# Performance work log

Hardware: AMD Instinct MI355X
Metric: run time of the kernel (lower is better)

The kernel has to match this reference:

```python
import jax, jax.numpy as jnp
import numpy as np

B, IN_DIM, T = 4, 512, 4096
EMBED, HEADS, NB_FEAT = 1024, 16, 256
D_HEAD = EMBED // HEADS
EPS = 1e-6


def _orthogonal_random_matrix(key, nb_rows, nb_cols):
    # scaling==1 branch: sqrt(nb_cols) * Q from reduced QR of a Gaussian block
    block = jax.random.normal(key, (nb_rows, nb_cols), dtype=jnp.float32)
    q, _ = jnp.linalg.qr(block)
    return jnp.sqrt(jnp.float32(nb_cols)) * q


def setup_inputs() -> dict:
    key = jax.random.key(0)
    kx, kq, kk, kv, ko, kp = jax.random.split(key, 6)
    s = 1.0 / np.sqrt(IN_DIM)
    return {
        "x": jax.random.normal(kx, (B, IN_DIM, T), dtype=jnp.float32),
        "Wq": jax.random.normal(kq, (IN_DIM, EMBED), dtype=jnp.float32) * s,
        "Wk": jax.random.normal(kk, (IN_DIM, EMBED), dtype=jnp.float32) * s,
        "Wv": jax.random.normal(kv, (IN_DIM, EMBED), dtype=jnp.float32) * s,
        "Wo": jax.random.normal(ko, (EMBED, EMBED), dtype=jnp.float32) * (1.0 / np.sqrt(EMBED)),
        "proj": _orthogonal_random_matrix(kp, NB_FEAT, D_HEAD),
    }


def reference(x, Wq, Wk, Wv, Wo, proj):
    b, c, t = x.shape
    x_bt = jnp.transpose(x, (0, 2, 1))  # (B, T, in_dim)
    Q = (x_bt @ Wq).reshape(b, t, HEADS, D_HEAD)
    K = (x_bt @ Wk).reshape(b, t, HEADS, D_HEAD)
    V = (x_bt @ Wv).reshape(b, t, HEADS, D_HEAD)
    # exponential random-feature map
    Qp = jnp.exp(jnp.einsum('bthd,fd->bthf', Q, proj)) + EPS
    Kp = jnp.exp(jnp.einsum('bthd,fd->bthf', K, proj)) + EPS
    K_sum = Kp.sum(axis=1)                              # (B, H, F)
    KV = jnp.einsum('bthf,bthd->bhfd', Kp, V)           # (B, H, F, D)
    denom = jnp.maximum(jnp.einsum('bthf,bhf->bth', Qp, K_sum), 1e-6)
    numer = jnp.einsum('bthf,bhfd->bthd', Qp, KV)
    attn = numer / denom[..., None]                     # (B, T, H, D)
    out2 = attn.reshape(b, t, HEADS * D_HEAD) @ Wo      # (B, T, embed)
    cat = jnp.concatenate([x_bt, out2], axis=-1)        # (B, T, in_dim+embed)
    return jnp.transpose(cat, (0, 2, 1))
```

## Files before the change

### kernel.cpp

```cpp
#include <hip/hip_runtime.h>


constexpr int kB  = 4;
constexpr int kIn = 512;
constexpr int kT  = 4096;
constexpr int kE  = 1024;
constexpr int kH  = 16;
constexpr int kD  = 64;
constexpr int kF  = 256;
constexpr int kQKVs = 3072;

typedef __attribute__((ext_vector_type(8))) short bf16x8;
typedef __attribute__((ext_vector_type(4))) float f32x4;

__device__ __forceinline__ unsigned short f2bf(float f) {
    unsigned u = __float_as_uint(f);
    u += 0x7fff + ((u >> 16) & 1);
    return (unsigned short)(u >> 16);
}
__device__ __forceinline__ float bf2f(unsigned short s) {
    return __uint_as_float(((unsigned)s) << 16);
}
__device__ __forceinline__ void gload_lds16(const void* g, void* l) {
    __builtin_amdgcn_global_load_lds((const __attribute__((address_space(1))) void*)g,
                                     (__attribute__((address_space(3))) void*)l, 16, 0, 0);
}

__global__ __launch_bounds__(256) void zero_kernel(float* __restrict__ p, int n) {
    int i = blockIdx.x * 256 + threadIdx.x;
    if (i < n) p[i] = 0.f;
}

__global__ __launch_bounds__(256) void copy_x_kernel(const float* __restrict__ x,
                                                     float* __restrict__ out) {
    const int perB4 = kIn * kT / 4;
    int idx = blockIdx.x * 256 + threadIdx.x;
    if (idx < kB * perB4) {
        int b = idx / perB4, e = idx % perB4;
        ((float4*)out)[(size_t)b * ((kIn + kE) * kT / 4) + e] = ((const float4*)x)[idx];
    }
}

__global__ __launch_bounds__(256) void f2b_flat_kernel(const float* __restrict__ s,
                                                       unsigned short* __restrict__ d, int n4) {
    int i = blockIdx.x * 256 + threadIdx.x;
    if (i < n4) {
        float4 v = ((const float4*)s)[i];
        ushort4 o;
        o.x = f2bf(v.x); o.y = f2bf(v.y); o.z = f2bf(v.z); o.w = f2bf(v.w);
        ((ushort4*)d)[i] = o;
    }
}

__global__ __launch_bounds__(256) void trans_f2b_kernel(const float* __restrict__ src,
                                                        unsigned short* __restrict__ dst,
                                                        int R, int C,
                                                        long sstride, long dstride) {
    __shared__ float L[64][68];
    src += (size_t)blockIdx.z * sstride;
    dst += (size_t)blockIdx.z * dstride;
    const int c0 = blockIdx.x * 64, r0 = blockIdx.y * 64;
    const int tid = threadIdx.x;
#pragma unroll
    for (int it = 0; it < 4; ++it) {
        int lin = it * 256 + tid;
        int i = lin >> 4;
        int j4 = (lin & 15) * 4;
        float4 v = *(const float4*)(src + (size_t)(r0 + i) * C + c0 + j4);
        L[j4 + 0][i] = v.x; L[j4 + 1][i] = v.y; L[j4 + 2][i] = v.z; L[j4 + 3][i] = v.w;
    }
    __syncthreads();
#pragma unroll
    for (int it = 0; it < 4; ++it) {
        int lin = it * 256 + tid;
        int cc = lin >> 4;
        int r4 = (lin & 15) * 4;
        ushort4 o;
        o.x = f2bf(L[cc][r4 + 0]); o.y = f2bf(L[cc][r4 + 1]);
        o.z = f2bf(L[cc][r4 + 2]); o.w = f2bf(L[cc][r4 + 3]);
        *(ushort4*)(dst + (size_t)(c0 + cc) * R + r0 + r4) = o;
    }
}

__global__ __launch_bounds__(256) void trans_qkv_kernel(const float* __restrict__ Wq,
                                                        const float* __restrict__ Wk,
                                                        const float* __restrict__ Wv,
                                                        unsigned short* __restrict__ dst) {
    __shared__ float L[64][68];
    const int z = blockIdx.z;
    const float* src = (z == 0) ? Wq : (z == 1) ? Wk : Wv;
    dst += (size_t)z * kE * kIn;
    const int c0 = blockIdx.x * 64, r0 = blockIdx.y * 64;
    const int tid = threadIdx.x;
#pragma unroll
    for (int it = 0; it < 4; ++it) {
        int lin = it * 256 + tid;
        int i = lin >> 4;
        int j4 = (lin & 15) * 4;
        float4 v = *(const float4*)(src + (size_t)(r0 + i) * kE + c0 + j4);
        L[j4 + 0][i] = v.x; L[j4 + 1][i] = v.y; L[j4 + 2][i] = v.z; L[j4 + 3][i] = v.w;
    }
    __syncthreads();
#pragma unroll
    for (int it = 0; it < 4; ++it) {
        int lin = it * 256 + tid;
        int cc = lin >> 4;
        int r4 = (lin & 15) * 4;
        ushort4 o;
        o.x = f2bf(L[cc][r4 + 0]); o.y = f2bf(L[cc][r4 + 1]);
        o.z = f2bf(L[cc][r4 + 2]); o.w = f2bf(L[cc][r4 + 3]);
        *(ushort4*)(dst + (size_t)(c0 + cc) * kIn + r0 + r4) = o;
    }
}

__device__ __forceinline__ void stage256(const unsigned short* __restrict__ A,
                                         const unsigned short* __restrict__ Bt,
                                         int K, int m0, int n0, int kt,
                                         unsigned short* AsB, unsigned short* BsB,
                                         int tid) {
    const int w = tid >> 6;
    const size_t k0 = (size_t)kt * 64;
#pragma unroll
    for (int r = 0; r < 4; ++r) {
        int idx = r * 512 + tid;
        int row = idx >> 3;
        int cg = (idx & 7) ^ (row & 7);
        gload_lds16(A + (size_t)(m0 + row) * K + k0 + cg * 8, AsB + r * 4096 + w * 512);
    }
#pragma unroll
    for (int r = 0; r < 4; ++r) {
        int idx = r * 512 + tid;
        int row = idx >> 3;
        int cg = (idx & 7) ^ (row & 7);
        gload_lds16(Bt + (size_t)(n0 + row) * K + k0 + cg * 8, BsB + r * 4096 + w * 512);
    }
}

__device__ __forceinline__ void gemm256_mainloop(const unsigned short* __restrict__ A,
                                                 const unsigned short* __restrict__ Bt,
                                                 int K, int m0, int n0,
                                                 unsigned short* smem,
                                                 f32x4 (&acc)[8][4]) {
    const int tid = threadIdx.x, lane = tid & 63, w = tid >> 6;
    const int col = lane & 15, quad = lane >> 4;
    const int wm = (w >> 2) * 128, wn = (w & 3) * 64;
    const int swz = col & 7;
    const int nt = K >> 6;
    unsigned short* As0 = smem;
    unsigned short* As1 = smem + 16384;
    unsigned short* Bs0 = smem + 32768;
    unsigned short* Bs1 = smem + 49152;

    stage256(A, Bt, K, m0, n0, 0, As0, Bs0, tid);
    stage256(A, Bt, K, m0, n0, 1, As1, Bs1, tid);
#pragma unroll
    for (int i = 0; i < 8; ++i)
#pragma unroll
        for (int j = 0; j < 4; ++j) acc[i][j] = (f32x4){0.f, 0.f, 0.f, 0.f};
    asm volatile("s_waitcnt vmcnt(8)" ::: "memory");
    __builtin_amdgcn_s_barrier();
    __builtin_amdgcn_sched_barrier(0);

    for (int t = 0; ; ++t) {
        const unsigned short* As_ = (t & 1) ? As1 : As0;
        const unsigned short* Bs_ = (t & 1) ? Bs1 : Bs0;
#pragma unroll
        for (int q = 0; q < 4; ++q) {
            const int ar0 = wm + (q >> 1) * 64;
            const int bc0 = wn + (q & 1) * 32;
            bf16x8 av[2][4], bv[2][2];
#pragma unroll
            for (int s = 0; s < 2; ++s) {
                const int kc = ((s * 4 + quad) ^ swz) * 8;
#pragma unroll
                for (int i = 0; i < 4; ++i)
                    av[s][i] = *(const bf16x8*)&As_[(ar0 + i * 16 + col) * 64 + kc];
#pragma unroll
                for (int j = 0; j < 2; ++j)
                    bv[s][j] = *(const bf16x8*)&Bs_[(bc0 + j * 16 + col) * 64 + kc];
            }
            __builtin_amdgcn_s_setprio(1);
#pragma unroll
            for (int s = 0; s < 2; ++s)
#pragma unroll
                for (int i = 0; i < 4; ++i)
#pragma unroll
                    for (int j = 0; j < 2; ++j)
                        acc[(q >> 1) * 4 + i][(q & 1) * 2 + j] =
                            __builtin_amdgcn_mfma_f32_16x16x32_bf16(
                                av[s][i], bv[s][j],
                                acc[(q >> 1) * 4 + i][(q & 1) * 2 + j], 0, 0, 0);
            __builtin_amdgcn_s_setprio(0);
            __builtin_amdgcn_sched_barrier(0);
            __builtin_amdgcn_s_barrier();
            __builtin_amdgcn_sched_barrier(0);
        }
        if (t == nt - 1) break;
        if (t + 2 < nt) {
            stage256(A, Bt, K, m0, n0, t + 2, (t & 1) ? As1 : As0, (t & 1) ? Bs1 : Bs0, tid);
            asm volatile("s_waitcnt vmcnt(8)" ::: "memory");
        } else {
            asm volatile("s_waitcnt vmcnt(0)" ::: "memory");
        }
        __builtin_amdgcn_sched_barrier(0);
        __builtin_amdgcn_s_barrier();
        __builtin_amdgcn_sched_barrier(0);
    }
}

__global__ __launch_bounds__(512) void gemm256_b16(const unsigned short* __restrict__ A,
                                                   const unsigned short* __restrict__ Bt,
                                                   unsigned short* __restrict__ C,
                                                   int N, int K, int ntN) {
    extern __shared__ unsigned short smem_us[];
    const int tid = threadIdx.x, lane = tid & 63, w = tid >> 6;
    const int col = lane & 15, quad = lane >> 4;
    const int wm = (w >> 2) * 128, wn = (w & 3) * 64;
    const int bid = blockIdx.x;
    const int qch = gridDim.x >> 3;
    const int swb = (bid & 7) * qch + (bid >> 3);
    const int mt = swb / ntN, ntl = swb - mt * ntN;
    const int m0 = mt * 256, n0 = ntl * 256;

    f32x4 acc[8][4];
    gemm256_mainloop(A, Bt, K, m0, n0, smem_us, acc);

    float* Tw = (float*)smem_us + w * 336;
    const int t2 = lane >> 2, n4 = (lane & 3) * 4;
#pragma unroll
    for (int ri = 0; ri < 8; ++ri)
#pragma unroll
        for (int cj = 0; cj < 4; ++cj) {
#pragma unroll
            for (int r = 0; r < 4; ++r)
                Tw[(quad * 4 + r) * 20 + col] = acc[ri][cj][r];
            float4 v = *(const float4*)&Tw[t2 * 20 + n4];
            ushort4 o;
            o.x = f2bf(v.x); o.y = f2bf(v.y); o.z = f2bf(v.z); o.w = f2bf(v.w);
            *(ushort4*)(C + (size_t)(m0 + wm + ri * 16 + t2) * N + n0 + wn + cj * 16 + n4) = o;
        }
}

__global__ __launch_bounds__(512) void gemm256_out(const unsigned short* __restrict__ A,
                                                   const unsigned short* __restrict__ Bt,
                                                   float* __restrict__ out,
                                                   int N, int K, int ntN) {
    extern __shared__ unsigned short smem_us[];
    const int tid = threadIdx.x, lane = tid & 63, w = tid >> 6;
    const int col = lane & 15, quad = lane >> 4;
    const int wm = (w >> 2) * 128, wn = (w & 3) * 64;
    const int bid = blockIdx.x;
    const int qch = gridDim.x >> 3;
    const int swb = (bid & 7) * qch + (bid >> 3);
    const int mt = swb / ntN, ntl = swb - mt * ntN;
    const int m0 = mt * 256, n0 = ntl * 256;

    f32x4 acc[8][4];
    gemm256_mainloop(A, Bt, K, m0, n0, smem_us, acc);

    const int b = m0 >> 12, t0 = m0 & 4095;
    float* dst = out + (size_t)b * (kIn + kE) * kT + (size_t)kIn * kT;
    float* Tw = (float*)smem_us + w * 336;
    const int n2 = lane >> 2, t4 = (lane & 3) * 4;
#pragma unroll
    for (int ri = 0; ri < 8; ++ri)
#pragma unroll
        for (int cj = 0; cj < 4; ++cj) {
            *(float4*)&Tw[col * 20 + quad * 4] =
                (float4){acc[ri][cj][0], acc[ri][cj][1], acc[ri][cj][2], acc[ri][cj][3]};
            float4 v = *(const float4*)&Tw[n2 * 20 + t4];
            *(float4*)(dst + (size_t)(n0 + wn + cj * 16 + n2) * kT + t0 + wm + ri * 16 + t4) = v;
        }
}

__global__ __launch_bounds__(256) void phaseA_mfma(const unsigned short* __restrict__ QKVb,
                                                   const unsigned short* __restrict__ projb,
                                                   float* __restrict__ KVg,
                                                   float* __restrict__ Ksumg) {
    __shared__ unsigned short Ks[64 * 64];
    __shared__ unsigned short VT[64 * 72];
    __shared__ unsigned short KpT[256 * 72];
    const int tid = threadIdx.x, lane = tid & 63, w = tid >> 6;
    const int col = lane & 15, quad = lane >> 4;
    const int bh = blockIdx.x, b = bh >> 4, h = bh & 15;
    const int grp = blockIdx.y;
    const int f0 = w * 64;
    const int swz = col & 7;

    bf16x8 bB[2][4];
#pragma unroll
    for (int s = 0; s < 2; ++s)
#pragma unroll
        for (int j = 0; j < 4; ++j)
            bB[s][j] = *(const bf16x8*)(projb + (size_t)(f0 + j * 16 + col) * 64 + s * 32 + quad * 8);

    f32x4 kvacc[4][4];
#pragma unroll
    for (int i = 0; i < 4; ++i)
#pragma unroll
        for (int j = 0; j < 4; ++j) kvacc[i][j] = (f32x4){0.f, 0.f, 0.f, 0.f};
    float ksum_acc[4] = {0.f, 0.f, 0.f, 0.f};

    for (int it = 0; it < 8; ++it) {
        const size_t rowbase = (size_t)(b * kT + grp * 512 + it * 64) * kQKVs + h * kD;
        __syncthreads();
#pragma unroll
        for (int i2 = 0; i2 < 2; ++i2) {
            int p = (i2 * 4 + w) * 64 + lane;
            int row = p >> 3;
            int cg = ((p & 7) ^ (row & 7)) * 8;
            gload_lds16(QKVb + rowbase + 1024 + (size_t)row * kQKVs + cg, &Ks[(i2 * 4 + w) * 512]);
        }
#pragma unroll
        for (int r = 0; r < 4; ++r) {
            int lin = r * 256 + tid;
            int t = lin >> 4, d4 = (lin & 15) * 4;
            ushort4 v = *(const ushort4*)(QKVb + rowbase + 2048 + (size_t)t * kQKVs + d4);
            VT[(d4 + 0) * 72 + t] = v.x; VT[(d4 + 1) * 72 + t] = v.y;
            VT[(d4 + 2) * 72 + t] = v.z; VT[(d4 + 3) * 72 + t] = v.w;
        }
        __syncthreads();
        bf16x8 av[2][4];
#pragma unroll
        for (int s = 0; s < 2; ++s)
#pragma unroll
            for (int i = 0; i < 4; ++i)
                av[s][i] = *(const bf16x8*)&Ks[(i * 16 + col) * 64 + ((s * 4 + quad) ^ swz) * 8];
#pragma unroll
        for (int j = 0; j < 4; ++j) {
            f32x4 sa[4];
#pragma unroll
            for (int i = 0; i < 4; ++i) sa[i] = (f32x4){0.f, 0.f, 0.f, 0.f};
#pragma unroll
            for (int s = 0; s < 2; ++s)
#pragma unroll
                for (int i = 0; i < 4; ++i)
                    sa[i] = __builtin_amdgcn_mfma_f32_16x16x32_bf16(av[s][i], bB[s][j], sa[i], 0, 0, 0);
            const int f = f0 + j * 16 + col;
#pragma unroll
            for (int i = 0; i < 4; ++i) {
                float e0 = __expf(sa[i][0]) + 1e-6f;
                float e1 = __expf(sa[i][1]) + 1e-6f;
                float e2 = __expf(sa[i][2]) + 1e-6f;
                float e3 = __expf(sa[i][3]) + 1e-6f;
                ksum_acc[j] += (e0 + e1) + (e2 + e3);
                ushort4 pk;
                pk.x = f2bf(e0); pk.y = f2bf(e1); pk.z = f2bf(e2); pk.w = f2bf(e3);
                *(ushort4*)&KpT[f * 72 + i * 16 + quad * 4] = pk;
            }
        }
#pragma unroll
        for (int s = 0; s < 2; ++s) {
            const int kc = s * 32 + quad * 8;
            bf16x8 a2[4], b2[4];
#pragma unroll
            for (int i = 0; i < 4; ++i)
                a2[i] = *(const bf16x8*)&KpT[(f0 + i * 16 + col) * 72 + kc];
#pragma unroll
            for (int jn = 0; jn < 4; ++jn)
                b2[jn] = *(const bf16x8*)&VT[(jn * 16 + col) * 72 + kc];
#pragma unroll
            for (int i = 0; i < 4; ++i)
#pragma unroll
                for (int jn = 0; jn < 4; ++jn)
                    kvacc[i][jn] = __builtin_amdgcn_mfma_f32_16x16x32_bf16(a2[i], b2[jn], kvacc[i][jn], 0, 0, 0);
        }
    }
    const size_t kvbase = (size_t)bh * (kF * kD);
#pragma unroll
    for (int i = 0; i < 4; ++i)
#pragma unroll
        for (int jn = 0; jn < 4; ++jn)
#pragma unroll
            for (int r = 0; r < 4; ++r)
                atomicAdd(&KVg[kvbase + (size_t)(f0 + i * 16 + quad * 4 + r) * kD + jn * 16 + col],
                          kvacc[i][jn][r]);
#pragma unroll
    for (int j = 0; j < 4; ++j) {
        float v = ksum_acc[j];
        v += __shfl_xor(v, 16);
        v += __shfl_xor(v, 32);
        if (quad == 0) atomicAdd(&Ksumg[(size_t)bh * kF + f0 + j * 16 + col], v);
    }
}

__global__ __launch_bounds__(256) void phaseB_mfma(const unsigned short* __restrict__ QKVb,
                                                   const unsigned short* __restrict__ projb,
                                                   const unsigned short* __restrict__ KVTb,
                                                   const float* __restrict__ Ksumg,
                                                   unsigned short* __restrict__ attnb) {
    __shared__ unsigned short Qs[64 * 64];
    __shared__ unsigned short Qp[64 * 264];
    __shared__ unsigned short KVTs[64 * 264];
    __shared__ float KsS[256];
    __shared__ float denp[4][64];
    const int tid = threadIdx.x, lane = tid & 63, w = tid >> 6;
    const int col = lane & 15, quad = lane >> 4;
    const int bh = blockIdx.x, b = bh >> 4, h = bh & 15;
    const int grp = blockIdx.y;
    const int f0 = w * 64;
    const int swz = col & 7;

    bf16x8 bB[2][4];
#pragma unroll
    for (int s = 0; s < 2; ++s)
#pragma unroll
        for (int j = 0; j < 4; ++j)
            bB[s][j] = *(const bf16x8*)(projb + (size_t)(f0 + j * 16 + col) * 64 + s * 32 + quad * 8);

#pragma unroll
    for (int r = 0; r < 8; ++r) {
        int lin = r * 256 + tid;
        int d = lin >> 5, fc8 = (lin & 31) * 8;
        *(bf16x8*)&KVTs[d * 264 + fc8] = *(const bf16x8*)(KVTb + (size_t)bh * 16384 + d * 256 + fc8);
    }
    KsS[tid] = Ksumg[(size_t)bh * kF + tid];

    for (int it = 0; it < 8; ++it) {
        const int tg0 = grp * 512 + it * 64;
        const size_t rowbase = (size_t)(b * kT + tg0) * kQKVs + h * kD;
        __syncthreads();
#pragma unroll
        for (int i2 = 0; i2 < 2; ++i2) {
            int p = (i2 * 4 + w) * 64 + lane;
            int row = p >> 3;
            int cg = ((p & 7) ^ (row & 7)) * 8;
            gload_lds16(QKVb + rowbase + (size_t)row * kQKVs + cg, &Qs[(i2 * 4 + w) * 512]);
        }
        __syncthreads();
        bf16x8 av[2][4];
#pragma unroll
        for (int s = 0; s < 2; ++s)
#pragma unroll
            for (int i = 0; i < 4; ++i)
                av[s][i] = *(const bf16x8*)&Qs[(i * 16 + col) * 64 + ((s * 4 + quad) ^ swz) * 8];
#pragma unroll
        for (int j = 0; j < 4; ++j) {
            f32x4 sa[4];
#pragma unroll
            for (int i = 0; i < 4; ++i) sa[i] = (f32x4){0.f, 0.f, 0.f, 0.f};
#pragma unroll
            for (int s = 0; s < 2; ++s)
#pragma unroll
                for (int i = 0; i < 4; ++i)
                    sa[i] = __builtin_amdgcn_mfma_f32_16x16x32_bf16(av[s][i], bB[s][j], sa[i], 0, 0, 0);
            const int f = f0 + j * 16 + col;
#pragma unroll
            for (int i = 0; i < 4; ++i) {
                const int tb = i * 16 + quad * 4;
                Qp[(tb + 0) * 264 + f] = f2bf(__expf(sa[i][0]) + 1e-6f);
                Qp[(tb + 1) * 264 + f] = f2bf(__expf(sa[i][1]) + 1e-6f);
                Qp[(tb + 2) * 264 + f] = f2bf(__expf(sa[i][2]) + 1e-6f);
                Qp[(tb + 3) * 264 + f] = f2bf(__expf(sa[i][3]) + 1e-6f);
            }
        }
        float dp = 0.f;
#pragma unroll
        for (int u = 0; u < 64; u += 8) {
            bf16x8 qv = *(const bf16x8*)&Qp[lane * 264 + f0 + u];
#pragma unroll
            for (int k2 = 0; k2 < 8; ++k2)
                dp += bf2f((unsigned short)qv[k2]) * KsS[f0 + u + k2];
        }
        denp[w][lane] = dp;
        __syncthreads();
        f32x4 nacc[4];
#pragma unroll
        for (int jn = 0; jn < 4; ++jn) nacc[jn] = (f32x4){0.f, 0.f, 0.f, 0.f};
#pragma unroll
        for (int s = 0; s < 8; ++s) {
            const int kc = s * 32 + quad * 8;
            bf16x8 aq = *(const bf16x8*)&Qp[(w * 16 + col) * 264 + kc];
#pragma unroll
            for (int jn = 0; jn < 4; ++jn) {
                bf16x8 bk = *(const bf16x8*)&KVTs[(jn * 16 + col) * 264 + kc];
                nacc[jn] = __builtin_amdgcn_mfma_f32_16x16x32_bf16(aq, bk, nacc[jn], 0, 0, 0);
            }
        }
#pragma unroll
        for (int r = 0; r < 4; ++r) {
            const int tl = w * 16 + quad * 4 + r;
            float den = denp[0][tl] + denp[1][tl] + denp[2][tl] + denp[3][tl];
            float rd = 1.f / fmaxf(den, 1e-6f);
            const size_t ob = (size_t)(b * kT + tg0 + tl) * kE + h * kD;
#pragma unroll
            for (int jn = 0; jn < 4; ++jn)
                attnb[ob + jn * 16 + col] = f2bf(nacc[jn][r] * rd);
        }
    }
}

extern "C" void kernel_launch(void* const* d_in, const int* in_sizes, int n_in,
                              void* d_out, int out_size, void* d_ws, size_t ws_size,
                              hipStream_t stream) {
    (void)in_sizes; (void)n_in; (void)out_size; (void)ws_size;
    const float* x    = (const float*)d_in[0];
    const float* Wq   = (const float*)d_in[1];
    const float* Wk   = (const float*)d_in[2];
    const float* Wv   = (const float*)d_in[3];
    const float* Wo   = (const float*)d_in[4];
    const float* proj = (const float*)d_in[5];
    float* out = (float*)d_out;

    static int attr_done = 0;
    if (!attr_done) {
        hipFuncSetAttribute((const void*)gemm256_b16,
                            hipFuncAttributeMaxDynamicSharedMemorySize, 131072);
        hipFuncSetAttribute((const void*)gemm256_out,
                            hipFuncAttributeMaxDynamicSharedMemorySize, 131072);
        attr_done = 1;
    }

    char* ws = (char*)d_ws;
    unsigned short* QKVb  = (unsigned short*)(ws);
    unsigned short* attnb = (unsigned short*)(ws + 100663296);
    unsigned short* Abuf  = (unsigned short*)(ws + 100663296);
    unsigned short* Btqkv = (unsigned short*)(ws + 134217728);
    unsigned short* WoT   = (unsigned short*)(ws + 137363456);
    unsigned short* projb = (unsigned short*)(ws + 139460608);
    float*          KVg   = (float*)(ws + 139493376);
    float*          Ksumg = (float*)(ws + 143687680);
    unsigned short* KVTb  = (unsigned short*)(ws + 143753216);

    copy_x_kernel<<<dim3(8192), 256, 0, stream>>>(x, out);

    trans_f2b_kernel<<<dim3(64, 8, 4), 256, 0, stream>>>(x, Abuf, kIn, kT,
                                                         (long)kIn * kT, (long)kT * kIn);
    trans_qkv_kernel<<<dim3(16, 8, 3), 256, 0, stream>>>(Wq, Wk, Wv, Btqkv);
    trans_f2b_kernel<<<dim3(16, 16, 1), 256, 0, stream>>>(Wo, WoT, kE, kE, 0, 0);
    f2b_flat_kernel<<<dim3(16), 256, 0, stream>>>(proj, projb, kF * kD / 4);

    gemm256_b16<<<dim3(768), 512, 131072, stream>>>(Abuf, Btqkv, QKVb, kQKVs, kIn, 12);

    const int nz = kB * kH * kF * kD + kB * kH * kF;
    zero_kernel<<<dim3((nz + 255) / 256), 256, 0, stream>>>(KVg, nz);

    phaseA_mfma<<<dim3(64, 8), 256, 0, stream>>>(QKVb, projb, KVg, Ksumg);
    trans_f2b_kernel<<<dim3(1, 4, 64), 256, 0, stream>>>(KVg, KVTb, kF, kD,
                                                         (long)kF * kD, (long)kF * kD);
    phaseB_mfma<<<dim3(64, 8), 256, 0, stream>>>(QKVb, projb, KVTb, Ksumg, attnb);

    gemm256_out<<<dim3(256), 512, 131072, stream>>>(attnb, WoT, out, kE, kE, 4);
}
```

Baseline: 371.8 us.

## Interleave GEMM global-to-LDS staging with MFMA phases in ping-pong schedule

The 256x256 bf16 GEMM main loop drops the separate stage-two-tiles-then-compute loop. In its place is a manually unrolled ping-pong schedule that spreads the global_load_lds copies for the next K tiles across eight MFMA sub-phases, each bracketed by barriers. Operand fragments are reorganised so each wave loads all four B fragments once per K step and reuses them across both M halves. The aim is to hide global memory latency and cut LDS reads. In exchange it adds more barriers, relies on carefully counted vmcnt waits, and assumes an even number of K tiles.

```diff
diff --git a/kernel.cpp b/kernel.cpp
--- a/kernel.cpp
+++ b/kernel.cpp
@@ -113,29 +113,6 @@
     }
 }
 
-__device__ __forceinline__ void stage256(const unsigned short* __restrict__ A,
-                                         const unsigned short* __restrict__ Bt,
-                                         int K, int m0, int n0, int kt,
-                                         unsigned short* AsB, unsigned short* BsB,
-                                         int tid) {
-    const int w = tid >> 6;
-    const size_t k0 = (size_t)kt * 64;
-#pragma unroll
-    for (int r = 0; r < 4; ++r) {
-        int idx = r * 512 + tid;
-        int row = idx >> 3;
-        int cg = (idx & 7) ^ (row & 7);
-        gload_lds16(A + (size_t)(m0 + row) * K + k0 + cg * 8, AsB + r * 4096 + w * 512);
-    }
-#pragma unroll
-    for (int r = 0; r < 4; ++r) {
-        int idx = r * 512 + tid;
-        int row = idx >> 3;
-        int cg = (idx & 7) ^ (row & 7);
-        gload_lds16(Bt + (size_t)(n0 + row) * K + k0 + cg * 8, BsB + r * 4096 + w * 512);
-    }
-}
-
 __device__ __forceinline__ void gemm256_mainloop(const unsigned short* __restrict__ A,
                                                  const unsigned short* __restrict__ Bt,
                                                  int K, int m0, int n0,
@@ -146,65 +123,125 @@
     const int wm = (w >> 2) * 128, wn = (w & 3) * 64;
     const int swz = col & 7;
     const int nt = K >> 6;
-    unsigned short* As0 = smem;
-    unsigned short* As1 = smem + 16384;
-    unsigned short* Bs0 = smem + 32768;
-    unsigned short* Bs1 = smem + 49152;
-
-    stage256(A, Bt, K, m0, n0, 0, As0, Bs0, tid);
-    stage256(A, Bt, K, m0, n0, 1, As1, Bs1, tid);
-#pragma unroll
-    for (int i = 0; i < 8; ++i)
-#pragma unroll
-        for (int j = 0; j < 4; ++j) acc[i][j] = (f32x4){0.f, 0.f, 0.f, 0.f};
-    asm volatile("s_waitcnt vmcnt(8)" ::: "memory");
-    __builtin_amdgcn_s_barrier();
-    __builtin_amdgcn_sched_barrier(0);
-
-    for (int t = 0; ; ++t) {
-        const unsigned short* As_ = (t & 1) ? As1 : As0;
-        const unsigned short* Bs_ = (t & 1) ? Bs1 : Bs0;
-#pragma unroll
-        for (int q = 0; q < 4; ++q) {
-            const int ar0 = wm + (q >> 1) * 64;
-            const int bc0 = wn + (q & 1) * 32;
-            bf16x8 av[2][4], bv[2][2];
-#pragma unroll
-            for (int s = 0; s < 2; ++s) {
-                const int kc = ((s * 4 + quad) ^ swz) * 8;
-#pragma unroll
-                for (int i = 0; i < 4; ++i)
-                    av[s][i] = *(const bf16x8*)&As_[(ar0 + i * 16 + col) * 64 + kc];
-#pragma unroll
-                for (int j = 0; j < 2; ++j)
-                    bv[s][j] = *(const bf16x8*)&Bs_[(bc0 + j * 16 + col) * 64 + kc];
-            }
-            __builtin_amdgcn_s_setprio(1);
-#pragma unroll
-            for (int s = 0; s < 2; ++s)
-#pragma unroll
-                for (int i = 0; i < 4; ++i)
-#pragma unroll
-                    for (int j = 0; j < 2; ++j)
-                        acc[(q >> 1) * 4 + i][(q & 1) * 2 + j] =
-                            __builtin_amdgcn_mfma_f32_16x16x32_bf16(
-                                av[s][i], bv[s][j],
-                                acc[(q >> 1) * 4 + i][(q & 1) * 2 + j], 0, 0, 0);
-            __builtin_amdgcn_s_setprio(0);
-            __builtin_amdgcn_sched_barrier(0);
-            __builtin_amdgcn_s_barrier();
-            __builtin_amdgcn_sched_barrier(0);
-        }
-        if (t == nt - 1) break;
-        if (t + 2 < nt) {
-            stage256(A, Bt, K, m0, n0, t + 2, (t & 1) ? As1 : As0, (t & 1) ? Bs1 : Bs0, tid);
-            asm volatile("s_waitcnt vmcnt(8)" ::: "memory");
-        } else {
-            asm volatile("s_waitcnt vmcnt(0)" ::: "memory");
-        }
+    const int L = (nt >> 1) - 1;
+
+    unsigned short* PA = smem;
+    unsigned short* QA = smem + 16384;
+    unsigned short* PB = smem + 32768;
+    unsigned short* QB = smem + 49152;
+
+    const int rowb = tid >> 3;
+    const int cgc = ((tid & 7) ^ (rowb & 7)) * 8;
+    const unsigned short* Ag = A + (size_t)(m0 + rowb) * K + cgc;
+    const unsigned short* Bg = Bt + (size_t)(n0 + rowb) * K + cgc;
+    unsigned short* PAw = PA + w * 512;
+    unsigned short* QAw = QA + w * 512;
+    unsigned short* PBw = PB + w * 512;
+    unsigned short* QBw = QB + w * 512;
+
+    auto stage = [&](const unsigned short* g, int kt, int r, unsigned short* lw) {
+        gload_lds16(g + (size_t)kt * 64 + (size_t)(r * 64) * K, lw + r * 4096);
+    };
+    auto sync_open = [&]() {
+        __builtin_amdgcn_sched_barrier(0);
+        __builtin_amdgcn_s_barrier();
+        asm volatile("s_waitcnt lgkmcnt(0)" ::: "memory");
+        __builtin_amdgcn_sched_barrier(0);
+    };
+    auto sync_close = [&]() {
         __builtin_amdgcn_sched_barrier(0);
         __builtin_amdgcn_s_barrier();
         __builtin_amdgcn_sched_barrier(0);
+    };
+
+    bf16x8 bv[2][4], av[4];
+    auto load_bv = [&](const unsigned short* Bbuf) {
+#pragma unroll
+        for (int s = 0; s < 2; ++s) {
+            const int kc = ((s * 4 + quad) ^ swz) * 8;
+#pragma unroll
+            for (int j = 0; j < 4; ++j)
+                bv[s][j] = *(const bf16x8*)&Bbuf[(wn + j * 16 + col) * 64 + kc];
+        }
+    };
+    auto load_av = [&](const unsigned short* Abuf, int mh, int s) {
+        const int kc = ((s * 4 + quad) ^ swz) * 8;
+#pragma unroll
+        for (int i4 = 0; i4 < 4; ++i4)
+            av[i4] = *(const bf16x8*)&Abuf[(wm + mh * 64 + i4 * 16 + col) * 64 + kc];
+    };
+    auto mfma_lo = [&](const bf16x8* bvr) {
+        __builtin_amdgcn_s_setprio(1);
+#pragma unroll
+        for (int i4 = 0; i4 < 4; ++i4)
+#pragma unroll
+            for (int j = 0; j < 4; ++j)
+                acc[i4][j] = __builtin_amdgcn_mfma_f32_16x16x32_bf16(av[i4], bvr[j], acc[i4][j], 0, 0, 0);
+        __builtin_amdgcn_s_setprio(0);
+    };
+    auto mfma_hi = [&](const bf16x8* bvr) {
+        __builtin_amdgcn_s_setprio(1);
+#pragma unroll
+        for (int i4 = 0; i4 < 4; ++i4)
+#pragma unroll
+            for (int j = 0; j < 4; ++j)
+                acc[4 + i4][j] = __builtin_amdgcn_mfma_f32_16x16x32_bf16(av[i4], bvr[j], acc[4 + i4][j], 0, 0, 0);
+        __builtin_amdgcn_s_setprio(0);
+    };
+
+#pragma unroll
+    for (int r = 0; r < 4; ++r) stage(Bg, 0, r, PBw);
+#pragma unroll
+    for (int r = 0; r < 4; ++r) stage(Ag, 0, r, PAw);
+#pragma unroll
+    for (int r = 0; r < 4; ++r) stage(Bg, 1, r, QBw);
+    stage(Ag, 1, 0, QAw);
+    stage(Ag, 1, 2, QAw);
+#pragma unroll
+    for (int i = 0; i < 8; ++i)
+#pragma unroll
+        for (int j = 0; j < 4; ++j) acc[i][j] = (f32x4){0.f, 0.f, 0.f, 0.f};
+    asm volatile("s_waitcnt vmcnt(6)" ::: "memory");
+    __builtin_amdgcn_s_barrier();
+    __builtin_amdgcn_sched_barrier(0);
+
+    for (int t = 0; t <= L; ++t) {
+        const bool more = (t < L);
+        const int ktA = 2 * t + 2, ktB = 2 * t + 3;
+        load_bv(PB);
+        load_av(PA, 0, 0);
+        stage(Ag, 2 * t + 1, 1, QAw);
+        stage(Ag, 2 * t + 1, 3, QAw);
+        sync_open(); mfma_lo(bv[0]); sync_close();
+        load_av(PA, 0, 1);
+        if (more) { stage(Bg, ktA, 0, PBw); stage(Bg, ktA, 1, PBw); }
+        sync_open(); mfma_lo(bv[1]); sync_close();
+        load_av(PA, 1, 0);
+        if (more) { stage(Bg, ktA, 2, PBw); stage(Bg, ktA, 3, PBw); }
+        sync_open(); mfma_hi(bv[0]); sync_close();
+        load_av(PA, 1, 1);
+        if (more) { stage(Ag, ktA, 0, PAw); stage(Ag, ktA, 2, PAw); }
+        sync_open(); mfma_hi(bv[1]);
+        __builtin_amdgcn_sched_barrier(0);
+        if (more) asm volatile("s_waitcnt vmcnt(6)" ::: "memory");
+        else      asm volatile("s_waitcnt vmcnt(0)" ::: "memory");
+        sync_close();
+        load_bv(QB);
+        load_av(QA, 0, 0);
+        if (more) { stage(Ag, ktA, 1, PAw); stage(Ag, ktA, 3, PAw); }
+        sync_open(); mfma_lo(bv[0]); sync_close();
+        load_av(QA, 0, 1);
+        if (more) { stage(Bg, ktB, 0, QBw); stage(Bg, ktB, 1, QBw); }
+        sync_open(); mfma_lo(bv[1]); sync_close();
+        load_av(QA, 1, 0);
+        if (more) { stage(Bg, ktB, 2, QBw); stage(Bg, ktB, 3, QBw); }
+        sync_open(); mfma_hi(bv[0]); sync_close();
+        load_av(QA, 1, 1);
+        if (more) { stage(Ag, ktB, 0, QAw); stage(Ag, ktB, 2, QAw); }
+        sync_open(); mfma_hi(bv[1]);
+        __builtin_amdgcn_sched_barrier(0);
+        if (more) asm volatile("s_waitcnt vmcnt(6)" ::: "memory");
+        sync_close();
     }
 }
 
```

After: 363.1 us. 2.3% less time.

## Replace 256x256 GEMM tiles with 128x256 tiles using K=32 double buffering

Applied to the files above, without the earlier changes.

Both projection GEMMs move from 256x256 output tiles with 64-deep K stages to 128x256 tiles with 32-deep K stages. Shared memory drops from 128KB dynamic to about 59KB static, and each wave holds a 4x4 accumulator instead of 8x4. The launch bound now asks for higher occupancy. The change aims to double the grid (1536 and 512 blocks) for better CU load balance. In exchange, it drops the XOR LDS swizzle, which risks bank conflicts, and gives up per-tile data reuse while adding one barrier per K step.

```diff
diff --git a/kernel.cpp b/kernel.cpp
--- a/kernel.cpp
+++ b/kernel.cpp
@@ -113,122 +113,94 @@
     }
 }
 
-__device__ __forceinline__ void stage256(const unsigned short* __restrict__ A,
-                                         const unsigned short* __restrict__ Bt,
-                                         int K, int m0, int n0, int kt,
-                                         unsigned short* AsB, unsigned short* BsB,
-                                         int tid) {
-    const int w = tid >> 6;
-    const size_t k0 = (size_t)kt * 64;
-#pragma unroll
-    for (int r = 0; r < 4; ++r) {
-        int idx = r * 512 + tid;
-        int row = idx >> 3;
-        int cg = (idx & 7) ^ (row & 7);
-        gload_lds16(A + (size_t)(m0 + row) * K + k0 + cg * 8, AsB + r * 4096 + w * 512);
-    }
-#pragma unroll
-    for (int r = 0; r < 4; ++r) {
-        int idx = r * 512 + tid;
-        int row = idx >> 3;
-        int cg = (idx & 7) ^ (row & 7);
-        gload_lds16(Bt + (size_t)(n0 + row) * K + k0 + cg * 8, BsB + r * 4096 + w * 512);
-    }
-}
-
-__device__ __forceinline__ void gemm256_mainloop(const unsigned short* __restrict__ A,
+__device__ __forceinline__ void gemm128_mainloop(const unsigned short* __restrict__ A,
                                                  const unsigned short* __restrict__ Bt,
                                                  int K, int m0, int n0,
-                                                 unsigned short* smem,
-                                                 f32x4 (&acc)[8][4]) {
+                                                 unsigned short* As, unsigned short* Bs,
+                                                 f32x4 (&acc)[4][4]) {
     const int tid = threadIdx.x, lane = tid & 63, w = tid >> 6;
     const int col = lane & 15, quad = lane >> 4;
-    const int wm = (w >> 2) * 128, wn = (w & 3) * 64;
-    const int swz = col & 7;
-    const int nt = K >> 6;
-    unsigned short* As0 = smem;
-    unsigned short* As1 = smem + 16384;
-    unsigned short* Bs0 = smem + 32768;
-    unsigned short* Bs1 = smem + 49152;
-
-    stage256(A, Bt, K, m0, n0, 0, As0, Bs0, tid);
-    stage256(A, Bt, K, m0, n0, 1, As1, Bs1, tid);
-#pragma unroll
-    for (int i = 0; i < 8; ++i)
+    const int wm = (w >> 2) * 64, wn = (w & 3) * 64;
+    const int nt = K >> 5;
+
+    const unsigned short* Agl  = A  + (size_t)(m0 + (tid >> 2)) * K + (tid & 3) * 8;
+    const unsigned short* Bgl0 = Bt + (size_t)(n0 + (tid >> 2)) * K + (tid & 3) * 8;
+    const unsigned short* Bgl1 = Bgl0 + (size_t)128 * K;
+    unsigned short* Asw = As + w * 512;
+    unsigned short* Bsw = Bs + w * 512;
+
+    auto stage = [&](int kt, int buf) {
+        gload_lds16(Agl  + kt * 32, Asw + buf * 4096);
+        gload_lds16(Bgl0 + kt * 32, Bsw + buf * 8192);
+        gload_lds16(Bgl1 + kt * 32, Bsw + buf * 8192 + 4096);
+    };
+
+#pragma unroll
+    for (int i = 0; i < 4; ++i)
 #pragma unroll
         for (int j = 0; j < 4; ++j) acc[i][j] = (f32x4){0.f, 0.f, 0.f, 0.f};
-    asm volatile("s_waitcnt vmcnt(8)" ::: "memory");
+
+    stage(0, 0);
+    if (nt > 1) stage(1, 1);
+    asm volatile("s_waitcnt vmcnt(3)" ::: "memory");
     __builtin_amdgcn_s_barrier();
     __builtin_amdgcn_sched_barrier(0);
 
-    for (int t = 0; ; ++t) {
-        const unsigned short* As_ = (t & 1) ? As1 : As0;
-        const unsigned short* Bs_ = (t & 1) ? Bs1 : Bs0;
-#pragma unroll
-        for (int q = 0; q < 4; ++q) {
-            const int ar0 = wm + (q >> 1) * 64;
-            const int bc0 = wn + (q & 1) * 32;
-            bf16x8 av[2][4], bv[2][2];
-#pragma unroll
-            for (int s = 0; s < 2; ++s) {
-                const int kc = ((s * 4 + quad) ^ swz) * 8;
-#pragma unroll
-                for (int i = 0; i < 4; ++i)
-                    av[s][i] = *(const bf16x8*)&As_[(ar0 + i * 16 + col) * 64 + kc];
-#pragma unroll
-                for (int j = 0; j < 2; ++j)
-                    bv[s][j] = *(const bf16x8*)&Bs_[(bc0 + j * 16 + col) * 64 + kc];
-            }
-            __builtin_amdgcn_s_setprio(1);
-#pragma unroll
-            for (int s = 0; s < 2; ++s)
-#pragma unroll
-                for (int i = 0; i < 4; ++i)
-#pragma unroll
-                    for (int j = 0; j < 2; ++j)
-                        acc[(q >> 1) * 4 + i][(q & 1) * 2 + j] =
-                            __builtin_amdgcn_mfma_f32_16x16x32_bf16(
-                                av[s][i], bv[s][j],
-                                acc[(q >> 1) * 4 + i][(q & 1) * 2 + j], 0, 0, 0);
-            __builtin_amdgcn_s_setprio(0);
+    for (int t = 0; t < nt; ++t) {
+        const int cur = t & 1;
+        const unsigned short* Ab = As + cur * 4096;
+        const unsigned short* Bb = Bs + cur * 8192;
+        bf16x8 av[4], bv[4];
+#pragma unroll
+        for (int i = 0; i < 4; ++i)
+            av[i] = *(const bf16x8*)&Ab[(wm + i * 16 + col) * 32 + quad * 8];
+#pragma unroll
+        for (int j = 0; j < 4; ++j)
+            bv[j] = *(const bf16x8*)&Bb[(wn + j * 16 + col) * 32 + quad * 8];
+        asm volatile("s_waitcnt lgkmcnt(0)" ::: "memory");
+        __builtin_amdgcn_sched_barrier(0);
+        __builtin_amdgcn_s_barrier();
+        if (t + 2 < nt) stage(t + 2, cur);
+        __builtin_amdgcn_sched_barrier(0);
+#pragma unroll
+        for (int i = 0; i < 4; ++i)
+#pragma unroll
+            for (int j = 0; j < 4; ++j)
+                acc[i][j] = __builtin_amdgcn_mfma_f32_16x16x32_bf16(av[i], bv[j], acc[i][j], 0, 0, 0);
+        if (t + 1 < nt) {
+            __builtin_amdgcn_sched_barrier(0);
+            if (t + 2 < nt) asm volatile("s_waitcnt vmcnt(3)" ::: "memory");
+            else            asm volatile("s_waitcnt vmcnt(0)" ::: "memory");
             __builtin_amdgcn_sched_barrier(0);
             __builtin_amdgcn_s_barrier();
             __builtin_amdgcn_sched_barrier(0);
         }
-        if (t == nt - 1) break;
-        if (t + 2 < nt) {
-            stage256(A, Bt, K, m0, n0, t + 2, (t & 1) ? As1 : As0, (t & 1) ? Bs1 : Bs0, tid);
-            asm volatile("s_waitcnt vmcnt(8)" ::: "memory");
-        } else {
-            asm volatile("s_waitcnt vmcnt(0)" ::: "memory");
-        }
-        __builtin_amdgcn_sched_barrier(0);
-        __builtin_amdgcn_s_barrier();
-        __builtin_amdgcn_sched_barrier(0);
-    }
-}
-
-__global__ __launch_bounds__(512) void gemm256_b16(const unsigned short* __restrict__ A,
-                                                   const unsigned short* __restrict__ Bt,
-                                                   unsigned short* __restrict__ C,
-                                                   int N, int K, int ntN) {
-    extern __shared__ unsigned short smem_us[];
+    }
+}
+
+__global__ __launch_bounds__(512, 4) void gemm128_b16(const unsigned short* __restrict__ A,
+                                                      const unsigned short* __restrict__ Bt,
+                                                      unsigned short* __restrict__ C,
+                                                      int N, int K, int ntN) {
+    __shared__ unsigned short As[2 * 4096];
+    __shared__ unsigned short Bs[2 * 8192];
+    __shared__ float Tt[8][336];
     const int tid = threadIdx.x, lane = tid & 63, w = tid >> 6;
     const int col = lane & 15, quad = lane >> 4;
-    const int wm = (w >> 2) * 128, wn = (w & 3) * 64;
+    const int wm = (w >> 2) * 64, wn = (w & 3) * 64;
     const int bid = blockIdx.x;
     const int qch = gridDim.x >> 3;
     const int swb = (bid & 7) * qch + (bid >> 3);
     const int mt = swb / ntN, ntl = swb - mt * ntN;
-    const int m0 = mt * 256, n0 = ntl * 256;
-
-    f32x4 acc[8][4];
-    gemm256_mainloop(A, Bt, K, m0, n0, smem_us, acc);
-
-    float* Tw = (float*)smem_us + w * 336;
+    const int m0 = mt * 128, n0 = ntl * 256;
+
+    f32x4 acc[4][4];
+    gemm128_mainloop(A, Bt, K, m0, n0, As, Bs, acc);
+
+    float* Tw = Tt[w];
     const int t2 = lane >> 2, n4 = (lane & 3) * 4;
 #pragma unroll
-    for (int ri = 0; ri < 8; ++ri)
+    for (int ri = 0; ri < 4; ++ri)
 #pragma unroll
         for (int cj = 0; cj < 4; ++cj) {
 #pragma unroll
@@ -241,29 +213,31 @@
         }
 }
 
-__global__ __launch_bounds__(512) void gemm256_out(const unsigned short* __restrict__ A,
-                                                   const unsigned short* __restrict__ Bt,
-                                                   float* __restrict__ out,
-                                                   int N, int K, int ntN) {
-    extern __shared__ unsigned short smem_us[];
+__global__ __launch_bounds__(512, 4) void gemm128_out(const unsigned short* __restrict__ A,
+                                                      const unsigned short* __restrict__ Bt,
+                                                      float* __restrict__ out,
+                                                      int N, int K, int ntN) {
+    __shared__ unsigned short As[2 * 4096];
+    __shared__ unsigned short Bs[2 * 8192];
+    __shared__ float Tt[8][336];
     const int tid = threadIdx.x, lane = tid & 63, w = tid >> 6;
     const int col = lane & 15, quad = lane >> 4;
-    const int wm = (w >> 2) * 128, wn = (w & 3) * 64;
+    const int wm = (w >> 2) * 64, wn = (w & 3) * 64;
     const int bid = blockIdx.x;
     const int qch = gridDim.x >> 3;
     const int swb = (bid & 7) * qch + (bid >> 3);
     const int mt = swb / ntN, ntl = swb - mt * ntN;
-    const int m0 = mt * 256, n0 = ntl * 256;
-
-    f32x4 acc[8][4];
-    gemm256_mainloop(A, Bt, K, m0, n0, smem_us, acc);
+    const int m0 = mt * 128, n0 = ntl * 256;
+
+    f32x4 acc[4][4];
+    gemm128_mainloop(A, Bt, K, m0, n0, As, Bs, acc);
 
     const int b = m0 >> 12, t0 = m0 & 4095;
     float* dst = out + (size_t)b * (kIn + kE) * kT + (size_t)kIn * kT;
-    float* Tw = (float*)smem_us + w * 336;
+    float* Tw = Tt[w];
     const int n2 = lane >> 2, t4 = (lane & 3) * 4;
 #pragma unroll
-    for (int ri = 0; ri < 8; ++ri)
+    for (int ri = 0; ri < 4; ++ri)
 #pragma unroll
         for (int cj = 0; cj < 4; ++cj) {
             *(float4*)&Tw[col * 20 + quad * 4] =
@@ -502,15 +476,6 @@
     const float* proj = (const float*)d_in[5];
     float* out = (float*)d_out;
 
-    static int attr_done = 0;
-    if (!attr_done) {
-        hipFuncSetAttribute((const void*)gemm256_b16,
-                            hipFuncAttributeMaxDynamicSharedMemorySize, 131072);
-        hipFuncSetAttribute((const void*)gemm256_out,
-                            hipFuncAttributeMaxDynamicSharedMemorySize, 131072);
-        attr_done = 1;
-    }
-
     char* ws = (char*)d_ws;
     unsigned short* QKVb  = (unsigned short*)(ws);
     unsigned short* attnb = (unsigned short*)(ws + 100663296);
@@ -530,7 +495,7 @@
     trans_f2b_kernel<<<dim3(16, 16, 1), 256, 0, stream>>>(Wo, WoT, kE, kE, 0, 0);
     f2b_flat_kernel<<<dim3(16), 256, 0, stream>>>(proj, projb, kF * kD / 4);
 
-    gemm256_b16<<<dim3(768), 512, 131072, stream>>>(Abuf, Btqkv, QKVb, kQKVs, kIn, 12);
+    gemm128_b16<<<dim3(1536), 512, 0, stream>>>(Abuf, Btqkv, QKVb, kQKVs, kIn, 12);
 
     const int nz = kB * kH * kF * kD + kB * kH * kF;
     zero_kernel<<<dim3((nz + 255) / 256), 256, 0, stream>>>(KVg, nz);
@@ -540,5 +505,5 @@
                                                          (long)kF * kD, (long)kF * kD);
     phaseB_mfma<<<dim3(64, 8), 256, 0, stream>>>(QKVb, projb, KVTb, Ksumg, attnb);
 
-    gemm256_out<<<dim3(256), 512, 131072, stream>>>(attnb, WoT, out, kE, kE, 4);
-}
+    gemm128_out<<<dim3(512), 512, 0, stream>>>(attnb, WoT, out, kE, kE, 4);
+}
```

Result: no change. 374.2 us (+0.7%).
